# Kernel tuning notes

Hardware: AMD Instinct MI355X
Metric: run time of the kernel (lower is better)

## Reference

```python
import jax, jax.numpy as jnp
import numpy as np
import math

B, N, DIM = 4, 2048, 768
HEADS, DIM_HEAD = 12, 64
SCALE = math.sqrt(DIM_HEAD)


def setup_inputs() -> dict:
    key = jax.random.key(0)
    ks = jax.random.split(key, 5)
    inner = HEADS * DIM_HEAD
    x = jax.random.normal(ks[0], (B, N, DIM), dtype=jnp.float32)
    # Linear weights stored as [in, out] so y = x @ W (equivalent to torch Linear with W.T)
    w_q = jax.random.normal(ks[1], (DIM, inner), dtype=jnp.float32) * 0.02
    w_k = jax.random.normal(ks[2], (DIM, inner), dtype=jnp.float32) * 0.02
    w_v = jax.random.normal(ks[3], (DIM, inner), dtype=jnp.float32) * 0.02
    w_o = jax.random.normal(ks[4], (inner, DIM), dtype=jnp.float32) * 0.02
    b_o = jnp.zeros((DIM,), dtype=jnp.float32)
    return {"x": x, "w_q": w_q, "w_k": w_k, "w_v": w_v, "w_o": w_o, "b_o": b_o}


def _split_heads(t):
    # [b, n, h*d] -> [b, h, n, d]
    b, n, _ = t.shape
    return t.reshape(b, n, HEADS, DIM_HEAD).transpose(0, 2, 1, 3)


def reference(x, w_q, w_k, w_v, w_o, b_o):
    # context = x (self-attention, kv_include_self=False)
    q = _split_heads(x @ w_q)  # [b,h,n,d]
    k = _split_heads(x @ w_k)
    v = _split_heads(x @ w_v)
    scores = jnp.einsum("bhnd,bhmd->bhnm", q, k) / SCALE  # [b,h,n,n]
    attn = jax.nn.softmax(scores, axis=-1)  # dropout p=0 -> identity
    h = jnp.einsum("bhnm,bhmd->bhnd", attn, v)  # [b,h,n,d]
    H = h.transpose(0, 2, 1, 3).reshape(x.shape[0], x.shape[1], HEADS * DIM_HEAD)
    out = H @ w_o + b_o
    return out
```

## Files before the change

kernel.cpp:

```cpp
#include <hip/hip_runtime.h>
#include <hip/hip_bf16.h>
#include <cstdint>
#include <cstddef>

#define HEADS 12
#define DHEAD 64
#define SEQ   2048
#define DIMM  768
#define BATCH 4
#define MROWS (BATCH*SEQ)
#define BH    (BATCH*HEADS)
#define SCL_Q 0.18033688011112042f

typedef __attribute__((ext_vector_type(8))) short short8;
typedef __attribute__((ext_vector_type(4))) short short4v;
typedef __attribute__((ext_vector_type(4))) float floatx4;

__device__ __forceinline__ unsigned short f2bf(float f) {
    union { float f; uint32_t u; } v; v.f = f;
    uint32_t u = v.u;
    u += 0x7fffu + ((u >> 16) & 1u);
    return (unsigned short)(u >> 16);
}
__device__ __forceinline__ float bf2f(unsigned short h) {
    union { uint32_t u; float f; } v; v.u = ((uint32_t)h) << 16;
    return v.f;
}
#if __has_builtin(__builtin_amdgcn_perm)
__device__ __forceinline__ uint32_t pkbf(float a, float b) {
    union { float f; uint32_t u; } ua, ub; ua.f = a; ub.f = b;
    return __builtin_amdgcn_perm(ub.u + 0x8000u, ua.u + 0x8000u, 0x07060302u);
}
#else
__device__ __forceinline__ uint32_t pkbf(float a, float b) {
    __hip_bfloat162 h = __float22bfloat162_rn(make_float2(a, b));
    uint32_t u; __builtin_memcpy(&u, &h, 4); return u;
}
#endif
__device__ __forceinline__ float fexp2(float x) {
#if __has_builtin(__builtin_amdgcn_exp2f)
    return __builtin_amdgcn_exp2f(x);
#else
    return exp2f(x);
#endif
}

#if __has_builtin(__builtin_amdgcn_global_load_lds)
#define HAVE_GLDS 1
__device__ __forceinline__ void glds16(const unsigned short* g, unsigned short* l) {
    __builtin_amdgcn_global_load_lds(
        (const __attribute__((address_space(1))) unsigned int*)g,
        (__attribute__((address_space(3))) unsigned int*)l, 16, 0, 0);
}
#else
#define HAVE_GLDS 0
#endif

__device__ __forceinline__ int detect_f32(const uint32_t* xw, int tid) {
    __shared__ int cnt_;
    if (tid == 0) cnt_ = 0;
    __syncthreads();
    uint32_t w = xw[(size_t)(tid & 255) * 4096];
    float av = fabsf(bf2f((unsigned short)(w & 0xFFFFu)));
    atomicAdd(&cnt_, (av >= 9.0949e-13f && av <= 256.0f) ? 1 : 0);
    __syncthreads();
    return (cnt_ < 192) ? 1 : 0;
}

__global__ __launch_bounds__(256) void prep(
    const void* __restrict__ x,
    const void* __restrict__ wq, const void* __restrict__ wk,
    const void* __restrict__ wv, const void* __restrict__ wo,
    unsigned short* __restrict__ xc,
    unsigned short* __restrict__ wtq, unsigned short* __restrict__ wtk,
    unsigned short* __restrict__ wtv, unsigned short* __restrict__ wto)
{
    const int tid = threadIdx.x;
    const int isf32 = detect_f32((const uint32_t*)x, tid);
    const int blk = blockIdx.x;

    if (blk < 2304) {
        __shared__ unsigned short tile[32][33];
        const int m = blk / 576, rr = blk % 576;
        const void* src; unsigned short* dst;
        switch (m) {
            case 0: src = wq; dst = wtq; break;
            case 1: src = wk; dst = wtk; break;
            case 2: src = wv; dst = wtv; break;
            default: src = wo; dst = wto; break;
        }
        const float* srcf = (const float*)src;
        const unsigned short* srcs = (const unsigned short*)src;
        const int tx = tid & 31, ty = tid >> 5;
        const int k0 = (rr % 24) * 32;
        const int n0 = (rr / 24) * 32;
        #pragma unroll
        for (int it = 0; it < 4; it++) {
            int r = ty + it * 8;
            size_t idx = (size_t)(k0 + r) * DIMM + n0 + tx;
            tile[r][tx] = isf32 ? f2bf(srcf[idx]) : srcs[idx];
        }
        __syncthreads();
        #pragma unroll
        for (int it = 0; it < 4; it++) {
            int r = ty + it * 8;
            dst[(size_t)(n0 + r) * DIMM + k0 + tx] = tile[tx][r];
        }
    } else {
        const size_t i0 = ((size_t)(blk - 2304) * 256 + tid) * 8;
        if (isf32) {
            const float* xf = (const float*)x;
            float4 a = *(const float4*)&xf[i0];
            float4 b = *(const float4*)&xf[i0 + 4];
            short8 s = { (short)f2bf(a.x), (short)f2bf(a.y), (short)f2bf(a.z), (short)f2bf(a.w),
                         (short)f2bf(b.x), (short)f2bf(b.y), (short)f2bf(b.z), (short)f2bf(b.w) };
            *(short8*)&xc[i0] = s;
        } else {
            *(short8*)&xc[i0] = *(const short8*)&((const unsigned short*)x)[i0];
        }
    }
}

__global__ __launch_bounds__(256) void gemm_qkv64(
    const unsigned short* __restrict__ A,
    const unsigned short* __restrict__ Wt0,
    const unsigned short* __restrict__ Wt1,
    const unsigned short* __restrict__ Wt2,
    unsigned short* __restrict__ OQ,
    unsigned short* __restrict__ OK,
    unsigned short* __restrict__ OVt)
{
    const int mode = blockIdx.z;
    const unsigned short* Wt = (mode == 1) ? Wt1 : (mode == 2) ? Wt2 : Wt0;

    __shared__ unsigned short As[128 * 64];
    __shared__ unsigned short Bs[64 * 64];

    const int tid  = threadIdx.x;
    const int wid  = tid >> 6;
    const int lane = tid & 63;
    const int l16  = lane & 15;
    const int quad = lane >> 4;
    const int wm   = wid & 1;
    const int wn   = wid >> 1;
    const int bm   = blockIdx.x * 128;
    const int bn   = blockIdx.y * 64;
    const bool swap = (mode != 2);

    floatx4 acc[8];
    #pragma unroll
    for (int i = 0; i < 8; i++) acc[i] = floatx4{0.f, 0.f, 0.f, 0.f};

    for (int kk = 0; kk < DIMM; kk += 64) {
        #pragma unroll
        for (int t = 0; t < 4; t++) {
            const int c  = t * 256 + tid;
            const int r  = c >> 3;
            const int lc = (((c & 7) ^ (r & 7))) * 8;
#if HAVE_GLDS
            glds16(&A[(size_t)(bm + r) * DIMM + kk + lc], &As[(t * 256 + wid * 64) * 8]);
#else
            *(short8*)&As[c * 8] = *(const short8*)&A[(size_t)(bm + r) * DIMM + kk + lc];
#endif
        }
        #pragma unroll
        for (int t = 0; t < 2; t++) {
            const int c  = t * 256 + tid;
            const int r  = c >> 3;
            const int lc = (((c & 7) ^ (r & 7))) * 8;
#if HAVE_GLDS
            glds16(&Wt[(size_t)(bn + r) * DIMM + kk + lc], &Bs[(t * 256 + wid * 64) * 8]);
#else
            *(short8*)&Bs[c * 8] = *(const short8*)&Wt[(size_t)(bn + r) * DIMM + kk + lc];
#endif
        }
        __syncthreads();
        #pragma unroll
        for (int ks = 0; ks < 2; ks++) {
            const int ph = ((ks * 4 + quad) ^ (l16 & 7)) * 8;
            short8 xa[4], wb[2];
            #pragma unroll
            for (int t = 0; t < 4; t++)
                xa[t] = *(const short8*)&As[(wm * 64 + t * 16 + l16) * 64 + ph];
            #pragma unroll
            for (int t = 0; t < 2; t++)
                wb[t] = *(const short8*)&Bs[(wn * 32 + t * 16 + l16) * 64 + ph];
            if (swap) {
                #pragma unroll
                for (int mt = 0; mt < 2; mt++)
                    #pragma unroll
                    for (int nt = 0; nt < 4; nt++)
                        acc[mt * 4 + nt] = __builtin_amdgcn_mfma_f32_16x16x32_bf16(
                            wb[mt], xa[nt], acc[mt * 4 + nt], 0, 0, 0);
            } else {
                #pragma unroll
                for (int mt = 0; mt < 4; mt++)
                    #pragma unroll
                    for (int nt = 0; nt < 2; nt++)
                        acc[mt * 2 + nt] = __builtin_amdgcn_mfma_f32_16x16x32_bf16(
                            xa[mt], wb[nt], acc[mt * 2 + nt], 0, 0, 0);
            }
        }
        __syncthreads();
    }

    if (swap) {
        unsigned short* Out = (mode == 0) ? OQ : OK;
        #pragma unroll
        for (int nt = 0; nt < 4; nt++) {
            const int grow = bm + wm * 64 + nt * 16 + l16;
            const int b = grow >> 11, n = grow & 2047;
            #pragma unroll
            for (int mt = 0; mt < 2; mt++) {
                const int gcol0 = bn + wn * 32 + mt * 16 + quad * 4;
                float v0 = acc[mt * 4 + nt][0], v1 = acc[mt * 4 + nt][1];
                float v2 = acc[mt * 4 + nt][2], v3 = acc[mt * 4 + nt][3];
                if (mode == 0) { v0 *= SCL_Q; v1 *= SCL_Q; v2 *= SCL_Q; v3 *= SCL_Q; }
                const int h = gcol0 >> 6, d = gcol0 & 63;
                size_t addr = ((size_t)(b * HEADS + h) * SEQ + n) * DHEAD + d;
                short4v pk = { (short)f2bf(v0), (short)f2bf(v1),
                               (short)f2bf(v2), (short)f2bf(v3) };
                *(short4v*)&Out[addr] = pk;
            }
        }
    } else {
        #pragma unroll
        for (int nt = 0; nt < 2; nt++) {
            const int gcol = bn + wn * 32 + nt * 16 + l16;
            const int h = gcol >> 6, d = gcol & 63;
            #pragma unroll
            for (int mt = 0; mt < 4; mt++) {
                const int grow0 = bm + wm * 64 + mt * 16 + quad * 4;
                const int b = grow0 >> 11, n0 = grow0 & 2047;
                size_t addr = ((size_t)(b * HEADS + h) * DHEAD + d) * SEQ + n0;
                short4v pk = { (short)f2bf(acc[mt * 2 + nt][0]), (short)f2bf(acc[mt * 2 + nt][1]),
                               (short)f2bf(acc[mt * 2 + nt][2]), (short)f2bf(acc[mt * 2 + nt][3]) };
                *(short4v*)&OVt[addr] = pk;
            }
        }
    }
}

__global__ __launch_bounds__(256) void gemm_o64(
    const unsigned short* __restrict__ A,
    const unsigned short* __restrict__ Wt,
    void* __restrict__ Out,
    const void* __restrict__ bias,
    const uint32_t* __restrict__ xsample)
{
    unsigned short* Out16 = (unsigned short*)Out;
    float* Outf           = (float*)Out;
    const int isf32 = detect_f32(xsample, threadIdx.x);

    __shared__ unsigned short As[128 * 64];
    __shared__ unsigned short Bs[64 * 64];

    const int tid  = threadIdx.x;
    const int wid  = tid >> 6;
    const int lane = tid & 63;
    const int l16  = lane & 15;
    const int quad = lane >> 4;
    const int wm   = wid & 1;
    const int wn   = wid >> 1;
    const int bm   = blockIdx.x * 128;
    const int bn   = blockIdx.y * 64;

    floatx4 acc[2][4];
    #pragma unroll
    for (int i = 0; i < 2; i++)
        #pragma unroll
        for (int j = 0; j < 4; j++)
            acc[i][j] = floatx4{0.f, 0.f, 0.f, 0.f};

    for (int kk = 0; kk < DIMM; kk += 64) {
        #pragma unroll
        for (int t = 0; t < 4; t++) {
            const int c  = t * 256 + tid;
            const int r  = c >> 3;
            const int lc = (((c & 7) ^ (r & 7))) * 8;
#if HAVE_GLDS
            glds16(&A[(size_t)(bm + r) * DIMM + kk + lc], &As[(t * 256 + wid * 64) * 8]);
#else
            *(short8*)&As[c * 8] = *(const short8*)&A[(size_t)(bm + r) * DIMM + kk + lc];
#endif
        }
        #pragma unroll
        for (int t = 0; t < 2; t++) {
            const int c  = t * 256 + tid;
            const int r  = c >> 3;
            const int lc = (((c & 7) ^ (r & 7))) * 8;
#if HAVE_GLDS
            glds16(&Wt[(size_t)(bn + r) * DIMM + kk + lc], &Bs[(t * 256 + wid * 64) * 8]);
#else
            *(short8*)&Bs[c * 8] = *(const short8*)&Wt[(size_t)(bn + r) * DIMM + kk + lc];
#endif
        }
        __syncthreads();
        #pragma unroll
        for (int ks = 0; ks < 2; ks++) {
            const int ph = ((ks * 4 + quad) ^ (l16 & 7)) * 8;
            short8 xa[4], wb[2];
            #pragma unroll
            for (int t = 0; t < 4; t++)
                xa[t] = *(const short8*)&As[(wm * 64 + t * 16 + l16) * 64 + ph];
            #pragma unroll
            for (int t = 0; t < 2; t++)
                wb[t] = *(const short8*)&Bs[(wn * 32 + t * 16 + l16) * 64 + ph];
            #pragma unroll
            for (int mt = 0; mt < 2; mt++)
                #pragma unroll
                for (int nt = 0; nt < 4; nt++)
                    acc[mt][nt] = __builtin_amdgcn_mfma_f32_16x16x32_bf16(
                        wb[mt], xa[nt], acc[mt][nt], 0, 0, 0);
        }
        __syncthreads();
    }

    #pragma unroll
    for (int nt = 0; nt < 4; nt++) {
        const int grow = bm + wm * 64 + nt * 16 + l16;
        #pragma unroll
        for (int mt = 0; mt < 2; mt++) {
            const int gcol0 = bn + wn * 32 + mt * 16 + quad * 4;
            const float v0 = acc[mt][nt][0], v1 = acc[mt][nt][1];
            const float v2 = acc[mt][nt][2], v3 = acc[mt][nt][3];
            if (isf32) {
                float4 bv = *(const float4*)&((const float*)bias)[gcol0];
                float4 o = { v0 + bv.x, v1 + bv.y, v2 + bv.z, v3 + bv.w };
                *(float4*)&Outf[(size_t)grow * DIMM + gcol0] = o;
            } else {
                const unsigned short* bb = &((const unsigned short*)bias)[gcol0];
                short4v pk = { (short)f2bf(v0 + bf2f(bb[0])),
                               (short)f2bf(v1 + bf2f(bb[1])),
                               (short)f2bf(v2 + bf2f(bb[2])),
                               (short)f2bf(v3 + bf2f(bb[3])) };
                *(short4v*)&Out16[(size_t)grow * DIMM + gcol0] = pk;
            }
        }
    }
}

__global__ __launch_bounds__(256, 3) void attn(
    const unsigned short* __restrict__ Q,
    const unsigned short* __restrict__ K,
    const unsigned short* __restrict__ Vt,
    unsigned short* __restrict__ Hout)
{
    __shared__ unsigned short KsB[2 * 64 * 64];
    __shared__ unsigned short VsB[2 * 64 * 64];
    __shared__ unsigned short Ps[8][16 * 64];

    const int tid  = threadIdx.x;
    const int wid  = tid >> 6;
    const int lane = tid & 63;
    const int l16  = lane & 15;
    const int quad = lane >> 4;
    const int sw   = l16 & 7;

    const int bh = blockIdx.x % BH;
    const int qt = blockIdx.x / BH;

    short8 qf[2][2];
    #pragma unroll
    for (int t = 0; t < 2; t++) {
        const int qrow = qt * 128 + wid * 32 + t * 16 + l16;
        const size_t qbase = ((size_t)bh * SEQ + qrow) * DHEAD;
        qf[t][0] = *(const short8*)&Q[qbase + quad * 8];
        qf[t][1] = *(const short8*)&Q[qbase + 32 + quad * 8];
    }

    const short8 ones = { (short)0x3F80, (short)0x3F80, (short)0x3F80, (short)0x3F80,
                          (short)0x3F80, (short)0x3F80, (short)0x3F80, (short)0x3F80 };

    floatx4 ot[2][4];
    floatx4 acc_l[2];
    #pragma unroll
    for (int t = 0; t < 2; t++) {
        acc_l[t] = floatx4{0.f, 0.f, 0.f, 0.f};
        #pragma unroll
        for (int i = 0; i < 4; i++) ot[t][i] = floatx4{0.f, 0.f, 0.f, 0.f};
    }

    const size_t kbase = (size_t)bh * SEQ * DHEAD;
    const size_t vbase = (size_t)bh * DHEAD * SEQ;

    short8 rk[2], rv[2];
    #pragma unroll
    for (int j = 0; j < 2; j++) {
        const int c = tid + j * 256, r = c >> 3, c8 = (c & 7) * 8;
        const int g = ((c & 7) ^ (r & 7)) * 8;
        short8 tk = *(const short8*)&K[kbase + (size_t)r * DHEAD + c8];
        short8 tv = *(const short8*)&Vt[vbase + (size_t)r * SEQ + c8];
        *(short8*)&KsB[r * 64 + g] = tk;
        *(short8*)&VsB[r * 64 + g] = tv;
        rk[j] = *(const short8*)&K[kbase + (size_t)(64 + r) * DHEAD + c8];
        rv[j] = *(const short8*)&Vt[vbase + (size_t)r * SEQ + 64 + c8];
    }

    short8 vfr[2][4];
    short8 pfr[2][2];

    for (int kt = 0; kt < SEQ / 64; kt++) {
        const int cur = kt & 1;
        unsigned short* Kc = &KsB[cur * 4096];
        unsigned short* Kn = &KsB[(cur ^ 1) * 4096];
        unsigned short* Vn = &VsB[(cur ^ 1) * 4096];

        if (kt > 0) {
            #pragma unroll
            for (int ks = 0; ks < 2; ks++) {
                #pragma unroll
                for (int dt = 0; dt < 4; dt++)
                    vfr[ks][dt] = *(const short8*)
                        &Vn[(dt * 16 + l16) * 64 + ((ks * 4 + quad) ^ sw) * 8];
                #pragma unroll
                for (int t = 0; t < 2; t++)
                    pfr[ks][t] = *(const short8*)
                        &Ps[wid * 2 + t][l16 * 64 + ((ks * 4 + quad) ^ sw) * 8];
            }
        }
        __syncthreads();

        if (kt + 1 < SEQ / 64) {
            #pragma unroll
            for (int j = 0; j < 2; j++) {
                const int c = tid + j * 256, r = c >> 3;
                const int g = ((c & 7) ^ (r & 7)) * 8;
                *(short8*)&Kn[r * 64 + g] = rk[j];
                *(short8*)&Vn[r * 64 + g] = rv[j];
            }
        }
        if (kt + 2 < SEQ / 64) {
            #pragma unroll
            for (int j = 0; j < 2; j++) {
                const int c = tid + j * 256, r = c >> 3, c8 = (c & 7) * 8;
                rk[j] = *(const short8*)&K[kbase + (size_t)((kt + 2) * 64 + r) * DHEAD + c8];
                rv[j] = *(const short8*)&Vt[vbase + (size_t)r * SEQ + (kt + 2) * 64 + c8];
            }
        }

        uint2 pk[2][4];
        #pragma unroll
        for (int mt = 0; mt < 4; mt++) {
            const int krow = (mt * 16 + l16) * 64;
            short8 kf0 = *(const short8*)&Kc[krow + (quad ^ sw) * 8];
            short8 kf1 = *(const short8*)&Kc[krow + ((4 + quad) ^ sw) * 8];
            #pragma unroll
            for (int t = 0; t < 2; t++) {
                floatx4 a = floatx4{0.f, 0.f, 0.f, 0.f};
                a = __builtin_amdgcn_mfma_f32_16x16x32_bf16(kf0, qf[t][0], a, 0, 0, 0);
                a = __builtin_amdgcn_mfma_f32_16x16x32_bf16(kf1, qf[t][1], a, 0, 0, 0);
                pk[t][mt] = (uint2){ pkbf(fexp2(a[0]), fexp2(a[1])),
                                     pkbf(fexp2(a[2]), fexp2(a[3])) };
            }
        }

        if (kt > 0) {
            __builtin_amdgcn_s_setprio(1);
            #pragma unroll
            for (int ks = 0; ks < 2; ks++) {
                #pragma unroll
                for (int t = 0; t < 2; t++) {
                    #pragma unroll
                    for (int dt = 0; dt < 4; dt++)
                        ot[t][dt] = __builtin_amdgcn_mfma_f32_16x16x32_bf16(
                            vfr[ks][dt], pfr[ks][t], ot[t][dt], 0, 0, 0);
                    acc_l[t] = __builtin_amdgcn_mfma_f32_16x16x32_bf16(
                        ones, pfr[ks][t], acc_l[t], 0, 0, 0);
                }
            }
            __builtin_amdgcn_s_setprio(0);
        }

        #pragma unroll
        for (int t = 0; t < 2; t++)
            #pragma unroll
            for (int mt = 0; mt < 4; mt++)
                *(uint2*)&Ps[wid * 2 + t]
                    [l16 * 64 + ((2 * mt + (quad >> 1)) ^ sw) * 8 + (quad & 1) * 4]
                    = pk[t][mt];
    }

    {
        unsigned short* Vl = &VsB[((SEQ / 64 - 1) & 1) * 4096];
        #pragma unroll
        for (int ks = 0; ks < 2; ks++) {
            #pragma unroll
            for (int dt = 0; dt < 4; dt++)
                vfr[ks][dt] = *(const short8*)
                    &Vl[(dt * 16 + l16) * 64 + ((ks * 4 + quad) ^ sw) * 8];
            #pragma unroll
            for (int t = 0; t < 2; t++)
                pfr[ks][t] = *(const short8*)
                    &Ps[wid * 2 + t][l16 * 64 + ((ks * 4 + quad) ^ sw) * 8];
        }
        __builtin_amdgcn_s_setprio(1);
        #pragma unroll
        for (int ks = 0; ks < 2; ks++)
            #pragma unroll
            for (int t = 0; t < 2; t++) {
                #pragma unroll
                for (int dt = 0; dt < 4; dt++)
                    ot[t][dt] = __builtin_amdgcn_mfma_f32_16x16x32_bf16(
                        vfr[ks][dt], pfr[ks][t], ot[t][dt], 0, 0, 0);
                acc_l[t] = __builtin_amdgcn_mfma_f32_16x16x32_bf16(
                    ones, pfr[ks][t], acc_l[t], 0, 0, 0);
            }
        __builtin_amdgcn_s_setprio(0);
    }

    const int b = bh / HEADS, h = bh % HEADS;
    #pragma unroll
    for (int t = 0; t < 2; t++) {
        const float inv_l = 1.0f / acc_l[t][0];
        unsigned short* Pw = Ps[wid * 2 + t];
        #pragma unroll
        for (int dt = 0; dt < 4; dt++) {
            uint2 pk2 = { pkbf(ot[t][dt][0] * inv_l, ot[t][dt][1] * inv_l),
                          pkbf(ot[t][dt][2] * inv_l, ot[t][dt][3] * inv_l) };
            *(uint2*)&Pw[l16 * 64 + ((2 * dt + (quad >> 1)) ^ sw) * 8 + (quad & 1) * 4]
                = pk2;
        }
        const int q_r   = lane >> 2;
        const int dpart = (lane & 3) * 16;
        const int rsw   = q_r & 7;
        short8 h0 = *(const short8*)&Pw[q_r * 64 + ((2 * (lane & 3)) ^ rsw) * 8];
        short8 h1 = *(const short8*)&Pw[q_r * 64 + ((2 * (lane & 3) + 1) ^ rsw) * 8];
        const int growg = b * SEQ + qt * 128 + wid * 32 + t * 16 + q_r;
        const size_t oaddr = (size_t)growg * DIMM + h * DHEAD + dpart;
        *(short8*)&Hout[oaddr] = h0;
        *(short8*)&Hout[oaddr + 8] = h1;
    }
}

extern "C" void kernel_launch(void* const* d_in, const int* in_sizes, int n_in,
                              void* d_out, int out_size, void* d_ws, size_t ws_size,
                              hipStream_t stream)
{
    (void)in_sizes; (void)n_in; (void)out_size;
    const void* x  = d_in[0];
    const void* wq = d_in[1];
    const void* wk = d_in[2];
    const void* wv = d_in[3];
    const void* wo = d_in[4];
    const void* bo = d_in[5];

    char* ws = (char*)d_ws;
    const size_t SZ_QKV = (size_t)MROWS * DIMM * sizeof(unsigned short);
    const size_t SZ_W   = (size_t)DIMM * DIMM * sizeof(unsigned short);
    const size_t need = 5 * SZ_QKV + 4 * SZ_W;
    if (ws_size < need) return;

    unsigned short* xc   = (unsigned short*)(ws);
    unsigned short* Qws  = (unsigned short*)(ws + 1 * SZ_QKV);
    unsigned short* Kws  = (unsigned short*)(ws + 2 * SZ_QKV);
    unsigned short* Vtws = (unsigned short*)(ws + 3 * SZ_QKV);
    unsigned short* Hws  = (unsigned short*)(ws + 4 * SZ_QKV);
    unsigned short* Wtq  = (unsigned short*)(ws + 5 * SZ_QKV);
    unsigned short* Wtk  = (unsigned short*)(ws + 5 * SZ_QKV + SZ_W);
    unsigned short* Wtv  = (unsigned short*)(ws + 5 * SZ_QKV + 2 * SZ_W);
    unsigned short* Wto  = (unsigned short*)(ws + 5 * SZ_QKV + 3 * SZ_W);

    hipLaunchKernelGGL(prep, dim3(2304 + MROWS * DIMM / 2048), dim3(256), 0, stream,
                       x, wq, wk, wv, wo, xc, Wtq, Wtk, Wtv, Wto);
    hipLaunchKernelGGL(gemm_qkv64, dim3(64, 12, 3), dim3(256), 0, stream,
                       xc, Wtq, Wtk, Wtv, Qws, Kws, Vtws);
    hipLaunchKernelGGL(attn, dim3(BH * (SEQ / 128)), dim3(256), 0, stream,
                       Qws, Kws, Vtws, Hws);
    hipLaunchKernelGGL(gemm_o64, dim3(64, 12), dim3(256), 0, stream,
                       Hws, Wto, d_out, bo, (const uint32_t*)x);
}
```

Baseline: 234.3 us.

## Fuse Q, K, V projection GEMMs into one kernel sharing the A tile

Each block now loads the shared input tile once and multiplies it against all three weight tiles, keeping three accumulator sets instead of launching a separate z-slice per projection. This removes the triple reload of the activation tile from global memory and cuts the grid from 2304 to 768 blocks. In exchange, register and LDS use per block roughly triple, with launch bounds asking for 3 waves per SIMD. The smaller grid may leave fewer blocks per CU for latency hiding.

```diff
diff --git a/kernel.cpp b/kernel.cpp
--- a/kernel.cpp
+++ b/kernel.cpp
@@ -121,20 +121,17 @@
     }
 }
 
-__global__ __launch_bounds__(256) void gemm_qkv64(
+__global__ __launch_bounds__(256, 3) void gemm_qkv_fused(
     const unsigned short* __restrict__ A,
-    const unsigned short* __restrict__ Wt0,
-    const unsigned short* __restrict__ Wt1,
-    const unsigned short* __restrict__ Wt2,
+    const unsigned short* __restrict__ Wq,
+    const unsigned short* __restrict__ Wk,
+    const unsigned short* __restrict__ Wv,
     unsigned short* __restrict__ OQ,
     unsigned short* __restrict__ OK,
     unsigned short* __restrict__ OVt)
 {
-    const int mode = blockIdx.z;
-    const unsigned short* Wt = (mode == 1) ? Wt1 : (mode == 2) ? Wt2 : Wt0;
-
     __shared__ unsigned short As[128 * 64];
-    __shared__ unsigned short Bs[64 * 64];
+    __shared__ unsigned short Bs[3][64 * 64];
 
     const int tid  = threadIdx.x;
     const int wid  = tid >> 6;
@@ -145,11 +142,15 @@
     const int wn   = wid >> 1;
     const int bm   = blockIdx.x * 128;
     const int bn   = blockIdx.y * 64;
-    const bool swap = (mode != 2);
-
-    floatx4 acc[8];
-    #pragma unroll
-    for (int i = 0; i < 8; i++) acc[i] = floatx4{0.f, 0.f, 0.f, 0.f};
+
+    floatx4 aqk[2][8];
+    floatx4 av[8];
+    #pragma unroll
+    for (int w = 0; w < 2; w++)
+        #pragma unroll
+        for (int i = 0; i < 8; i++) aqk[w][i] = floatx4{0.f, 0.f, 0.f, 0.f};
+    #pragma unroll
+    for (int i = 0; i < 8; i++) av[i] = floatx4{0.f, 0.f, 0.f, 0.f};
 
     for (int kk = 0; kk < DIMM; kk += 64) {
         #pragma unroll
@@ -168,44 +169,58 @@
             const int c  = t * 256 + tid;
             const int r  = c >> 3;
             const int lc = (((c & 7) ^ (r & 7))) * 8;
+            const size_t goff = (size_t)(bn + r) * DIMM + kk + lc;
+            const int loff = (t * 256 + wid * 64) * 8;
 #if HAVE_GLDS
-            glds16(&Wt[(size_t)(bn + r) * DIMM + kk + lc], &Bs[(t * 256 + wid * 64) * 8]);
-#else
-            *(short8*)&Bs[c * 8] = *(const short8*)&Wt[(size_t)(bn + r) * DIMM + kk + lc];
+            glds16(&Wq[goff], &Bs[0][loff]);
+            glds16(&Wk[goff], &Bs[1][loff]);
+            glds16(&Wv[goff], &Bs[2][loff]);
+#else
+            *(short8*)&Bs[0][c * 8] = *(const short8*)&Wq[goff];
+            *(short8*)&Bs[1][c * 8] = *(const short8*)&Wk[goff];
+            *(short8*)&Bs[2][c * 8] = *(const short8*)&Wv[goff];
 #endif
         }
         __syncthreads();
         #pragma unroll
         for (int ks = 0; ks < 2; ks++) {
             const int ph = ((ks * 4 + quad) ^ (l16 & 7)) * 8;
-            short8 xa[4], wb[2];
+            short8 xa[4];
             #pragma unroll
             for (int t = 0; t < 4; t++)
                 xa[t] = *(const short8*)&As[(wm * 64 + t * 16 + l16) * 64 + ph];
             #pragma unroll
-            for (int t = 0; t < 2; t++)
-                wb[t] = *(const short8*)&Bs[(wn * 32 + t * 16 + l16) * 64 + ph];
-            if (swap) {
+            for (int w = 0; w < 2; w++) {
+                short8 wb[2];
+                #pragma unroll
+                for (int t = 0; t < 2; t++)
+                    wb[t] = *(const short8*)&Bs[w][(wn * 32 + t * 16 + l16) * 64 + ph];
                 #pragma unroll
                 for (int mt = 0; mt < 2; mt++)
                     #pragma unroll
                     for (int nt = 0; nt < 4; nt++)
-                        acc[mt * 4 + nt] = __builtin_amdgcn_mfma_f32_16x16x32_bf16(
-                            wb[mt], xa[nt], acc[mt * 4 + nt], 0, 0, 0);
-            } else {
+                        aqk[w][mt * 4 + nt] = __builtin_amdgcn_mfma_f32_16x16x32_bf16(
+                            wb[mt], xa[nt], aqk[w][mt * 4 + nt], 0, 0, 0);
+            }
+            {
+                short8 wb[2];
+                #pragma unroll
+                for (int t = 0; t < 2; t++)
+                    wb[t] = *(const short8*)&Bs[2][(wn * 32 + t * 16 + l16) * 64 + ph];
                 #pragma unroll
                 for (int mt = 0; mt < 4; mt++)
                     #pragma unroll
                     for (int nt = 0; nt < 2; nt++)
-                        acc[mt * 2 + nt] = __builtin_amdgcn_mfma_f32_16x16x32_bf16(
-                            xa[mt], wb[nt], acc[mt * 2 + nt], 0, 0, 0);
+                        av[mt * 2 + nt] = __builtin_amdgcn_mfma_f32_16x16x32_bf16(
+                            xa[mt], wb[nt], av[mt * 2 + nt], 0, 0, 0);
             }
         }
         __syncthreads();
     }
 
-    if (swap) {
-        unsigned short* Out = (mode == 0) ? OQ : OK;
+    #pragma unroll
+    for (int w = 0; w < 2; w++) {
+        unsigned short* Out = (w == 0) ? OQ : OK;
         #pragma unroll
         for (int nt = 0; nt < 4; nt++) {
             const int grow = bm + wm * 64 + nt * 16 + l16;
@@ -213,9 +228,9 @@
             #pragma unroll
             for (int mt = 0; mt < 2; mt++) {
                 const int gcol0 = bn + wn * 32 + mt * 16 + quad * 4;
-                float v0 = acc[mt * 4 + nt][0], v1 = acc[mt * 4 + nt][1];
-                float v2 = acc[mt * 4 + nt][2], v3 = acc[mt * 4 + nt][3];
-                if (mode == 0) { v0 *= SCL_Q; v1 *= SCL_Q; v2 *= SCL_Q; v3 *= SCL_Q; }
+                float v0 = aqk[w][mt * 4 + nt][0], v1 = aqk[w][mt * 4 + nt][1];
+                float v2 = aqk[w][mt * 4 + nt][2], v3 = aqk[w][mt * 4 + nt][3];
+                if (w == 0) { v0 *= SCL_Q; v1 *= SCL_Q; v2 *= SCL_Q; v3 *= SCL_Q; }
                 const int h = gcol0 >> 6, d = gcol0 & 63;
                 size_t addr = ((size_t)(b * HEADS + h) * SEQ + n) * DHEAD + d;
                 short4v pk = { (short)f2bf(v0), (short)f2bf(v1),
@@ -223,20 +238,19 @@
                 *(short4v*)&Out[addr] = pk;
             }
         }
-    } else {
-        #pragma unroll
-        for (int nt = 0; nt < 2; nt++) {
-            const int gcol = bn + wn * 32 + nt * 16 + l16;
-            const int h = gcol >> 6, d = gcol & 63;
-            #pragma unroll
-            for (int mt = 0; mt < 4; mt++) {
-                const int grow0 = bm + wm * 64 + mt * 16 + quad * 4;
-                const int b = grow0 >> 11, n0 = grow0 & 2047;
-                size_t addr = ((size_t)(b * HEADS + h) * DHEAD + d) * SEQ + n0;
-                short4v pk = { (short)f2bf(acc[mt * 2 + nt][0]), (short)f2bf(acc[mt * 2 + nt][1]),
-                               (short)f2bf(acc[mt * 2 + nt][2]), (short)f2bf(acc[mt * 2 + nt][3]) };
-                *(short4v*)&OVt[addr] = pk;
-            }
+    }
+    #pragma unroll
+    for (int nt = 0; nt < 2; nt++) {
+        const int gcol = bn + wn * 32 + nt * 16 + l16;
+        const int h = gcol >> 6, d = gcol & 63;
+        #pragma unroll
+        for (int mt = 0; mt < 4; mt++) {
+            const int grow0 = bm + wm * 64 + mt * 16 + quad * 4;
+            const int b = grow0 >> 11, n0 = grow0 & 2047;
+            size_t addr = ((size_t)(b * HEADS + h) * DHEAD + d) * SEQ + n0;
+            short4v pk = { (short)f2bf(av[mt * 2 + nt][0]), (short)f2bf(av[mt * 2 + nt][1]),
+                           (short)f2bf(av[mt * 2 + nt][2]), (short)f2bf(av[mt * 2 + nt][3]) };
+            *(short4v*)&OVt[addr] = pk;
         }
     }
 }
@@ -563,7 +577,7 @@
 
     hipLaunchKernelGGL(prep, dim3(2304 + MROWS * DIMM / 2048), dim3(256), 0, stream,
                        x, wq, wk, wv, wo, xc, Wtq, Wtk, Wtv, Wto);
-    hipLaunchKernelGGL(gemm_qkv64, dim3(64, 12, 3), dim3(256), 0, stream,
+    hipLaunchKernelGGL(gemm_qkv_fused, dim3(64, 12), dim3(256), 0, stream,
                        xc, Wtq, Wtk, Wtv, Qws, Kws, Vtws);
     hipLaunchKernelGGL(attn, dim3(BH * (SEQ / 128)), dim3(256), 0, stream,
                        Qws, Kws, Vtws, Hws);
```

Result: faster. 220.7 us (median of 2 runs) (-5.8%).
